# Optimization experiments

Hardware: AMD Instinct MI355X
Metric: run time of the kernel (lower is better)

Reference implementation:

```python
import jax, jax.numpy as jnp
import numpy as np

N = 8192
E = 131072
D_IN = 128
D_OUT = 128
EPS = 1e-5


def setup_inputs() -> dict:
    key = jax.random.key(0)
    k1, k2, k3, k4 = jax.random.split(key, 4)
    x = jax.random.normal(k1, (N, D_IN), dtype=jnp.float32)
    edge_index = jax.random.randint(k2, (2, E), 0, N, dtype=jnp.int64)
    weight = jax.random.normal(k3, (D_IN, D_OUT), dtype=jnp.float32)
    bias = jax.random.normal(k4, (D_OUT,), dtype=jnp.float32)
    return {"x": x, "edge_index": edge_index, "weight": weight, "bias": bias}


def reference(x, edge_index, weight, bias):
    n = x.shape[0]
    row, col = edge_index[0], edge_index[1]
    # dense adjacency build, exactly as the torch module does
    adj = jnp.zeros((n, n), dtype=x.dtype).at[row, col].set(1.0)
    adj = jnp.maximum(adj, adj.T)                      # symmetrize
    adj = adj + jnp.eye(n, dtype=x.dtype)              # self-loops (added, may yield 2 on diag)
    d_inv_sqrt = 1.0 / jnp.sqrt(adj.sum(axis=1) + EPS)  # [N]
    # D^{-1/2} A D^{-1/2} via broadcasting (same math as diag matmuls)
    norm_adj = d_inv_sqrt[:, None] * adj * d_inv_sqrt[None, :]
    out = norm_adj @ x            # [N, D_IN] aggregation
    out = out @ weight + bias     # [N, D_OUT]
    return out
```

## Files before the change

### kernel.cpp

```cpp
#include <hip/hip_runtime.h>
#include <stdint.h>

#define N_NODES 8192
#define NE      131072
#define DCH     128
#define WPR     256
#define MAXDEG  128
#define ZROW    8192
#define EPS     1e-5f

__global__ __launch_bounds__(256) void edge_kernel(const void* __restrict__ ei_raw,
                                                   uint32_t* __restrict__ bm) {
    int lane = threadIdx.x & 63;
    const long long* p64 = (const long long*)ei_raw;
    const int*       p32 = (const int*)ei_raw;
    bool is64 = __all((unsigned long long)p64[lane] < (unsigned long long)N_NODES);
    int e = blockIdx.x * 256 + threadIdx.x;
    int r, c;
    if (is64) { r = (int)p64[e]; c = (int)p64[NE + e]; }
    else      { r = p32[e];      c = p32[NE + e]; }
    atomicOr(&bm[r * WPR + (c >> 5)], 1u << (c & 31));
    atomicOr(&bm[c * WPR + (r >> 5)], 1u << (r & 31));
}

__global__ __launch_bounds__(256) void extract_kernel(const uint4* __restrict__ bm4,
                                                      float* __restrict__ dinv,
                                                      int* __restrict__ cnts,
                                                      uint16_t* __restrict__ nbr,
                                                      float* __restrict__ y) {
    if (blockIdx.x == 0 && threadIdx.x < DCH)
        y[(size_t)ZROW * DCH + threadIdx.x] = 0.0f;

    int lane = threadIdx.x & 63;
    int node = blockIdx.x * 4 + (threadIdx.x >> 6);
    uint4 w = bm4[(size_t)node * 64 + lane];
    int c = __popc(w.x) + __popc(w.y) + __popc(w.z) + __popc(w.w);
    int pre = c;
    #pragma unroll
    for (int d = 1; d < 64; d <<= 1) {
        int v = __shfl_up(pre, d);
        if (lane >= d) pre += v;
    }
    int tot  = __shfl(pre, 63);
    int excl = pre - c;
    int cnt  = tot > MAXDEG ? MAXDEG : tot;
    int kpad = (cnt + 7) & ~7;
    if (lane == 0) {
        dinv[node] = 1.0f / sqrtf((float)tot + 1.0f + EPS);
        cnts[node] = kpad;
    }
    uint32_t wd[4] = {w.x, w.y, w.z, w.w};
    int basebit = lane * 128;
    int o = excl;
    #pragma unroll
    for (int m = 0; m < 4; ++m) {
        uint32_t v = wd[m];
        while (v) {
            int b = __ffs(v) - 1; v &= v - 1;
            if (o < MAXDEG) nbr[(size_t)node * MAXDEG + o] = (uint16_t)(basebit + m * 32 + b);
            ++o;
        }
    }
    int p = cnt + lane;
    if (p < kpad) nbr[(size_t)node * MAXDEG + p] = (uint16_t)ZROW;
}

__global__ __launch_bounds__(256) void gemm_kernel(const float* __restrict__ X,
                                                   const float* __restrict__ W,
                                                   const float* __restrict__ dinv,
                                                   float* __restrict__ y) {
    __shared__ float sA[64][132];
    int t = threadIdx.x;
    int row0 = blockIdx.x * 64;
    int col0 = blockIdx.y * 64;
    {
        int k4 = t & 31;
        int r  = t >> 5;
        #pragma unroll
        for (int p = 0; p < 8; ++p) {
            float4 v = *(const float4*)&X[(size_t)(row0 + r + p * 8) * DCH + k4 * 4];
            *(float4*)&sA[r + p * 8][k4 * 4] = v;
        }
    }
    __syncthreads();

    int tx = t & 15, ty = t >> 4;
    int cg = col0 + tx * 4;
    int r0 = ty * 4;
    float acc[4][4] = {};
    #pragma unroll 4
    for (int k = 0; k < DCH; ++k) {
        float4 w = *(const float4*)&W[(size_t)k * DCH + cg];
        float a0 = sA[r0 + 0][k];
        float a1 = sA[r0 + 1][k];
        float a2 = sA[r0 + 2][k];
        float a3 = sA[r0 + 3][k];
        acc[0][0] += a0 * w.x; acc[0][1] += a0 * w.y; acc[0][2] += a0 * w.z; acc[0][3] += a0 * w.w;
        acc[1][0] += a1 * w.x; acc[1][1] += a1 * w.y; acc[1][2] += a1 * w.z; acc[1][3] += a1 * w.w;
        acc[2][0] += a2 * w.x; acc[2][1] += a2 * w.y; acc[2][2] += a2 * w.z; acc[2][3] += a2 * w.w;
        acc[3][0] += a3 * w.x; acc[3][1] += a3 * w.y; acc[3][2] += a3 * w.z; acc[3][3] += a3 * w.w;
    }
    #pragma unroll
    for (int i = 0; i < 4; ++i) {
        float d = dinv[row0 + r0 + i];
        float4 o;
        o.x = d * acc[i][0]; o.y = d * acc[i][1]; o.z = d * acc[i][2]; o.w = d * acc[i][3];
        *(float4*)&y[(size_t)(row0 + r0 + i) * DCH + cg] = o;
    }
}

__global__ __launch_bounds__(256) void aggregate_kernel(const uint16_t* __restrict__ nbr,
                                                        const float* __restrict__ dinv,
                                                        const int* __restrict__ cnts,
                                                        const float* __restrict__ y,
                                                        const float* __restrict__ bias,
                                                        float* __restrict__ out) {
    __shared__ uint32_t s_list[4][64];
    int w    = threadIdx.x >> 6;
    int lane = threadIdx.x & 63;
    int node = blockIdx.x * 4 + w;

    s_list[w][lane] = ((const uint32_t*)nbr)[(size_t)node * (MAXDEG / 2) + lane];
    const uint16_t* sl = (const uint16_t*)s_list[w];

    int   kpad = __builtin_amdgcn_readfirstlane(cnts[node]);
    float di   = dinv[node];
    const float2* y2 = (const float2*)y;

    float2 a0 = y2[(size_t)node * 64 + lane];
    float2 a1 = {0, 0}, a2 = {0, 0}, a3 = {0, 0};
    float2 a4 = {0, 0}, a5 = {0, 0}, a6 = {0, 0}, a7 = {0, 0};

    for (int k = 0; k < kpad; k += 8) {
        int j0 = __builtin_amdgcn_readfirstlane((int)sl[k + 0]);
        int j1 = __builtin_amdgcn_readfirstlane((int)sl[k + 1]);
        int j2 = __builtin_amdgcn_readfirstlane((int)sl[k + 2]);
        int j3 = __builtin_amdgcn_readfirstlane((int)sl[k + 3]);
        int j4 = __builtin_amdgcn_readfirstlane((int)sl[k + 4]);
        int j5 = __builtin_amdgcn_readfirstlane((int)sl[k + 5]);
        int j6 = __builtin_amdgcn_readfirstlane((int)sl[k + 6]);
        int j7 = __builtin_amdgcn_readfirstlane((int)sl[k + 7]);
        float2 q0 = y2[(size_t)j0 * 64 + lane];
        float2 q1 = y2[(size_t)j1 * 64 + lane];
        float2 q2 = y2[(size_t)j2 * 64 + lane];
        float2 q3 = y2[(size_t)j3 * 64 + lane];
        float2 q4 = y2[(size_t)j4 * 64 + lane];
        float2 q5 = y2[(size_t)j5 * 64 + lane];
        float2 q6 = y2[(size_t)j6 * 64 + lane];
        float2 q7 = y2[(size_t)j7 * 64 + lane];
        a0.x += q0.x; a0.y += q0.y;  a1.x += q1.x; a1.y += q1.y;
        a2.x += q2.x; a2.y += q2.y;  a3.x += q3.x; a3.y += q3.y;
        a4.x += q4.x; a4.y += q4.y;  a5.x += q5.x; a5.y += q5.y;
        a6.x += q6.x; a6.y += q6.y;  a7.x += q7.x; a7.y += q7.y;
    }

    float2 bb = ((const float2*)bias)[lane];
    float2 r;
    r.x = di * (((a0.x + a1.x) + (a2.x + a3.x)) + ((a4.x + a5.x) + (a6.x + a7.x))) + bb.x;
    r.y = di * (((a0.y + a1.y) + (a2.y + a3.y)) + ((a4.y + a5.y) + (a6.y + a7.y))) + bb.y;
    ((float2*)out)[(size_t)node * 64 + lane] = r;
}

extern "C" void kernel_launch(void* const* d_in, const int* in_sizes, int n_in,
                              void* d_out, int out_size, void* d_ws, size_t ws_size,
                              hipStream_t stream) {
    const float* xp  = (const float*)d_in[0];
    const void*  eip = d_in[1];
    const float* Wp  = (const float*)d_in[2];
    const float* bp  = (const float*)d_in[3];
    float*       op  = (float*)d_out;

    uint8_t* ws = (uint8_t*)d_ws;
    uint32_t* bmp   = (uint32_t*)ws;
    float*    dinvp = (float*)   (ws + (size_t)8 * 1024 * 1024);
    int*      cntp  = (int*)     (ws + (size_t)8 * 1024 * 1024 + 32 * 1024);
    uint16_t* nbrp  = (uint16_t*)(ws + (size_t)8 * 1024 * 1024 + 64 * 1024);
    float*    yp    = (float*)   (ws + (size_t)10 * 1024 * 1024 + 64 * 1024);

    hipMemsetAsync(bmp, 0, (size_t)N_NODES * WPR * sizeof(uint32_t), stream);
    edge_kernel<<<NE / 256, 256, 0, stream>>>(eip, bmp);
    extract_kernel<<<N_NODES / 4, 256, 0, stream>>>((const uint4*)bmp, dinvp, cntp, nbrp, yp);
    gemm_kernel<<<dim3(N_NODES / 64, 2), 256, 0, stream>>>(xp, Wp, dinvp, yp);
    aggregate_kernel<<<N_NODES / 4, 256, 0, stream>>>(nbrp, dinvp, cntp, yp, bp, op);
}
```

Before: 105.4 us.

## Fuse edge build with GEMM and fold neighbor extraction into aggregation

Edge scatter and the X@W GEMM now run in one launch, with disjoint block ranges, so they can overlap. Degrees are counted with atomics when a bit is newly set. The separate extract kernel is removed: aggregation reads the bitmap row, builds the neighbor list in shared memory and scales each neighbor by its own inverse sqrt degree. This cuts two launches and the nbr/dinv round trips, at the cost of extra degree atomics and per-neighbor degree loads and sqrt in the gather loop.

Result: slower. 118.4 us (+12.3%).

```diff
diff --git a/kernel.cpp b/kernel.cpp
--- a/kernel.cpp
+++ b/kernel.cpp
@@ -5,159 +5,137 @@
 #define NE      131072
 #define DCH     128
 #define WPR     256
-#define MAXDEG  128
-#define ZROW    8192
+#define MAXC    128
 #define EPS     1e-5f
 
-__global__ __launch_bounds__(256) void edge_kernel(const void* __restrict__ ei_raw,
-                                                   uint32_t* __restrict__ bm) {
-    int lane = threadIdx.x & 63;
-    const long long* p64 = (const long long*)ei_raw;
-    const int*       p32 = (const int*)ei_raw;
-    bool is64 = __all((unsigned long long)p64[lane] < (unsigned long long)N_NODES);
-    int e = blockIdx.x * 256 + threadIdx.x;
-    int r, c;
-    if (is64) { r = (int)p64[e]; c = (int)p64[NE + e]; }
-    else      { r = p32[e];      c = p32[NE + e]; }
-    atomicOr(&bm[r * WPR + (c >> 5)], 1u << (c & 31));
-    atomicOr(&bm[c * WPR + (r >> 5)], 1u << (r & 31));
+__global__ __launch_bounds__(256) void build_gemm_kernel(
+    const void*  __restrict__ ei_raw,
+    const float* __restrict__ X,
+    const float* __restrict__ W,
+    uint32_t* __restrict__ bm,
+    int*      __restrict__ deg,
+    float*    __restrict__ z)
+{
+    int t = threadIdx.x;
+    if (blockIdx.x < 512) {
+        int lane = t & 63;
+        const long long* p64 = (const long long*)ei_raw;
+        const int*       p32 = (const int*)ei_raw;
+        bool is64 = __all((unsigned long long)p64[lane] < (unsigned long long)N_NODES);
+        int e = blockIdx.x * 256 + t;
+        int r, c;
+        if (is64) { r = (int)p64[e]; c = (int)p64[NE + e]; }
+        else      { r = p32[e];      c = p32[NE + e]; }
+        uint32_t mc = 1u << (c & 31), mr = 1u << (r & 31);
+        uint32_t o1 = atomicOr(&bm[r * WPR + (c >> 5)], mc);
+        if (!(o1 & mc)) atomicAdd(&deg[r], 1);
+        uint32_t o2 = atomicOr(&bm[c * WPR + (r >> 5)], mr);
+        if (!(o2 & mr)) atomicAdd(&deg[c], 1);
+    } else {
+        __shared__ float sA[64][132];
+        int bx = blockIdx.x - 512;
+        int row0 = (bx >> 1) * 64;
+        int col0 = (bx & 1) * 64;
+        {
+            int k4 = t & 31;
+            int r  = t >> 5;
+            #pragma unroll
+            for (int p = 0; p < 8; ++p) {
+                float4 v = *(const float4*)&X[(size_t)(row0 + r + p * 8) * DCH + k4 * 4];
+                *(float4*)&sA[r + p * 8][k4 * 4] = v;
+            }
+        }
+        __syncthreads();
+        int tx = t & 15, ty = t >> 4;
+        int cg = col0 + tx * 4;
+        int r0 = ty * 4;
+        float acc[4][4] = {};
+        #pragma unroll 4
+        for (int k = 0; k < DCH; ++k) {
+            float4 w = *(const float4*)&W[(size_t)k * DCH + cg];
+            float a0 = sA[r0 + 0][k];
+            float a1 = sA[r0 + 1][k];
+            float a2 = sA[r0 + 2][k];
+            float a3 = sA[r0 + 3][k];
+            acc[0][0] += a0 * w.x; acc[0][1] += a0 * w.y; acc[0][2] += a0 * w.z; acc[0][3] += a0 * w.w;
+            acc[1][0] += a1 * w.x; acc[1][1] += a1 * w.y; acc[1][2] += a1 * w.z; acc[1][3] += a1 * w.w;
+            acc[2][0] += a2 * w.x; acc[2][1] += a2 * w.y; acc[2][2] += a2 * w.z; acc[2][3] += a2 * w.w;
+            acc[3][0] += a3 * w.x; acc[3][1] += a3 * w.y; acc[3][2] += a3 * w.z; acc[3][3] += a3 * w.w;
+        }
+        #pragma unroll
+        for (int i = 0; i < 4; ++i) {
+            float4 o;
+            o.x = acc[i][0]; o.y = acc[i][1]; o.z = acc[i][2]; o.w = acc[i][3];
+            *(float4*)&z[(size_t)(row0 + r0 + i) * DCH + cg] = o;
+        }
+    }
 }
 
-__global__ __launch_bounds__(256) void extract_kernel(const uint4* __restrict__ bm4,
-                                                      float* __restrict__ dinv,
-                                                      int* __restrict__ cnts,
-                                                      uint16_t* __restrict__ nbr,
-                                                      float* __restrict__ y) {
-    if (blockIdx.x == 0 && threadIdx.x < DCH)
-        y[(size_t)ZROW * DCH + threadIdx.x] = 0.0f;
+__global__ __launch_bounds__(256) void aggregate_kernel(
+    const uint4* __restrict__ bm4,
+    const int*   __restrict__ deg,
+    const float* __restrict__ z,
+    const float* __restrict__ bias,
+    float*       __restrict__ out)
+{
+    __shared__ uint16_t slist[4][MAXC];
+    int w    = threadIdx.x >> 6;
+    int lane = threadIdx.x & 63;
+    int node = blockIdx.x * 4 + w;
 
-    int lane = threadIdx.x & 63;
-    int node = blockIdx.x * 4 + (threadIdx.x >> 6);
-    uint4 w = bm4[(size_t)node * 64 + lane];
-    int c = __popc(w.x) + __popc(w.y) + __popc(w.z) + __popc(w.w);
+    uint4 b = bm4[(size_t)node * 64 + lane];
+    int c = __popc(b.x) + __popc(b.y) + __popc(b.z) + __popc(b.w);
     int pre = c;
     #pragma unroll
     for (int d = 1; d < 64; d <<= 1) {
         int v = __shfl_up(pre, d);
         if (lane >= d) pre += v;
     }
-    int tot  = __shfl(pre, 63);
-    int excl = pre - c;
-    int cnt  = tot > MAXDEG ? MAXDEG : tot;
-    int kpad = (cnt + 7) & ~7;
-    if (lane == 0) {
-        dinv[node] = 1.0f / sqrtf((float)tot + 1.0f + EPS);
-        cnts[node] = kpad;
-    }
-    uint32_t wd[4] = {w.x, w.y, w.z, w.w};
-    int basebit = lane * 128;
-    int o = excl;
-    #pragma unroll
-    for (int m = 0; m < 4; ++m) {
-        uint32_t v = wd[m];
-        while (v) {
-            int b = __ffs(v) - 1; v &= v - 1;
-            if (o < MAXDEG) nbr[(size_t)node * MAXDEG + o] = (uint16_t)(basebit + m * 32 + b);
-            ++o;
+    int total = __shfl(pre, 63);
+    int excl  = pre - c;
+
+    {
+        uint32_t wd[4] = {b.x, b.y, b.z, b.w};
+        int basebit = lane * 128;
+        int o = excl;
+        #pragma unroll
+        for (int m = 0; m < 4; ++m) {
+            uint32_t v = wd[m];
+            while (v) {
+                int bb = __ffs(v) - 1; v &= v - 1;
+                if (o < MAXC) slist[w][o] = (uint16_t)(basebit + m * 32 + bb);
+                ++o;
+            }
         }
     }
-    int p = cnt + lane;
-    if (p < kpad) nbr[(size_t)node * MAXDEG + p] = (uint16_t)ZROW;
-}
+    int cap  = total > MAXC ? MAXC : total;
+    int kpad = (cap + 7) & ~7;
+    int p = cap + lane;
+    if (p < kpad) slist[w][p] = (uint16_t)node;
 
-__global__ __launch_bounds__(256) void gemm_kernel(const float* __restrict__ X,
-                                                   const float* __restrict__ W,
-                                                   const float* __restrict__ dinv,
-                                                   float* __restrict__ y) {
-    __shared__ float sA[64][132];
-    int t = threadIdx.x;
-    int row0 = blockIdx.x * 64;
-    int col0 = blockIdx.y * 64;
-    {
-        int k4 = t & 31;
-        int r  = t >> 5;
-        #pragma unroll
-        for (int p = 0; p < 8; ++p) {
-            float4 v = *(const float4*)&X[(size_t)(row0 + r + p * 8) * DCH + k4 * 4];
-            *(float4*)&sA[r + p * 8][k4 * 4] = v;
-        }
-    }
-    __syncthreads();
+    const float2* z2 = (const float2*)z;
+    float dn = 1.0f / sqrtf((float)total + 1.0f + EPS);
 
-    int tx = t & 15, ty = t >> 4;
-    int cg = col0 + tx * 4;
-    int r0 = ty * 4;
-    float acc[4][4] = {};
-    #pragma unroll 4
-    for (int k = 0; k < DCH; ++k) {
-        float4 w = *(const float4*)&W[(size_t)k * DCH + cg];
-        float a0 = sA[r0 + 0][k];
-        float a1 = sA[r0 + 1][k];
-        float a2 = sA[r0 + 2][k];
-        float a3 = sA[r0 + 3][k];
-        acc[0][0] += a0 * w.x; acc[0][1] += a0 * w.y; acc[0][2] += a0 * w.z; acc[0][3] += a0 * w.w;
-        acc[1][0] += a1 * w.x; acc[1][1] += a1 * w.y; acc[1][2] += a1 * w.z; acc[1][3] += a1 * w.w;
-        acc[2][0] += a2 * w.x; acc[2][1] += a2 * w.y; acc[2][2] += a2 * w.z; acc[2][3] += a2 * w.w;
-        acc[3][0] += a3 * w.x; acc[3][1] += a3 * w.y; acc[3][2] += a3 * w.z; acc[3][3] += a3 * w.w;
-    }
-    #pragma unroll
-    for (int i = 0; i < 4; ++i) {
-        float d = dinv[row0 + r0 + i];
-        float4 o;
-        o.x = d * acc[i][0]; o.y = d * acc[i][1]; o.z = d * acc[i][2]; o.w = d * acc[i][3];
-        *(float4*)&y[(size_t)(row0 + r0 + i) * DCH + cg] = o;
-    }
-}
-
-__global__ __launch_bounds__(256) void aggregate_kernel(const uint16_t* __restrict__ nbr,
-                                                        const float* __restrict__ dinv,
-                                                        const int* __restrict__ cnts,
-                                                        const float* __restrict__ y,
-                                                        const float* __restrict__ bias,
-                                                        float* __restrict__ out) {
-    __shared__ uint32_t s_list[4][64];
-    int w    = threadIdx.x >> 6;
-    int lane = threadIdx.x & 63;
-    int node = blockIdx.x * 4 + w;
-
-    s_list[w][lane] = ((const uint32_t*)nbr)[(size_t)node * (MAXDEG / 2) + lane];
-    const uint16_t* sl = (const uint16_t*)s_list[w];
-
-    int   kpad = __builtin_amdgcn_readfirstlane(cnts[node]);
-    float di   = dinv[node];
-    const float2* y2 = (const float2*)y;
-
-    float2 a0 = y2[(size_t)node * 64 + lane];
-    float2 a1 = {0, 0}, a2 = {0, 0}, a3 = {0, 0};
-    float2 a4 = {0, 0}, a5 = {0, 0}, a6 = {0, 0}, a7 = {0, 0};
+    float2 self = z2[(size_t)node * 64 + lane];
+    float2 a0, a1 = {0,0}, a2 = {0,0}, a3 = {0,0}, a4 = {0,0}, a5 = {0,0}, a6 = {0,0}, a7 = {0,0};
+    a0.x = dn * self.x; a0.y = dn * self.y;
 
     for (int k = 0; k < kpad; k += 8) {
-        int j0 = __builtin_amdgcn_readfirstlane((int)sl[k + 0]);
-        int j1 = __builtin_amdgcn_readfirstlane((int)sl[k + 1]);
-        int j2 = __builtin_amdgcn_readfirstlane((int)sl[k + 2]);
-        int j3 = __builtin_amdgcn_readfirstlane((int)sl[k + 3]);
-        int j4 = __builtin_amdgcn_readfirstlane((int)sl[k + 4]);
-        int j5 = __builtin_amdgcn_readfirstlane((int)sl[k + 5]);
-        int j6 = __builtin_amdgcn_readfirstlane((int)sl[k + 6]);
-        int j7 = __builtin_amdgcn_readfirstlane((int)sl[k + 7]);
-        float2 q0 = y2[(size_t)j0 * 64 + lane];
-        float2 q1 = y2[(size_t)j1 * 64 + lane];
-        float2 q2 = y2[(size_t)j2 * 64 + lane];
-        float2 q3 = y2[(size_t)j3 * 64 + lane];
-        float2 q4 = y2[(size_t)j4 * 64 + lane];
-        float2 q5 = y2[(size_t)j5 * 64 + lane];
-        float2 q6 = y2[(size_t)j6 * 64 + lane];
-        float2 q7 = y2[(size_t)j7 * 64 + lane];
-        a0.x += q0.x; a0.y += q0.y;  a1.x += q1.x; a1.y += q1.y;
-        a2.x += q2.x; a2.y += q2.y;  a3.x += q3.x; a3.y += q3.y;
-        a4.x += q4.x; a4.y += q4.y;  a5.x += q5.x; a5.y += q5.y;
-        a6.x += q6.x; a6.y += q6.y;  a7.x += q7.x; a7.y += q7.y;
+        #define STEP(i, AX) {                                                        \
+            int idx = k + i;                                                         \
+            int j = __builtin_amdgcn_readfirstlane((int)slist[w][idx]);              \
+            float dj = (idx < cap) ? 1.0f / sqrtf((float)deg[j] + 1.0f + EPS) : 0.f; \
+            float2 q = z2[(size_t)j * 64 + lane];                                    \
+            AX.x += dj * q.x; AX.y += dj * q.y; }
+        STEP(0, a0) STEP(1, a1) STEP(2, a2) STEP(3, a3)
+        STEP(4, a4) STEP(5, a5) STEP(6, a6) STEP(7, a7)
+        #undef STEP
     }
 
     float2 bb = ((const float2*)bias)[lane];
     float2 r;
-    r.x = di * (((a0.x + a1.x) + (a2.x + a3.x)) + ((a4.x + a5.x) + (a6.x + a7.x))) + bb.x;
-    r.y = di * (((a0.y + a1.y) + (a2.y + a3.y)) + ((a4.y + a5.y) + (a6.y + a7.y))) + bb.y;
+    r.x = dn * (((a0.x + a1.x) + (a2.x + a3.x)) + ((a4.x + a5.x) + (a6.x + a7.x))) + bb.x;
+    r.y = dn * (((a0.y + a1.y) + (a2.y + a3.y)) + ((a4.y + a5.y) + (a6.y + a7.y))) + bb.y;
     ((float2*)out)[(size_t)node * 64 + lane] = r;
 }
 
@@ -171,15 +149,11 @@
     float*       op  = (float*)d_out;
 
     uint8_t* ws = (uint8_t*)d_ws;
-    uint32_t* bmp   = (uint32_t*)ws;
-    float*    dinvp = (float*)   (ws + (size_t)8 * 1024 * 1024);
-    int*      cntp  = (int*)     (ws + (size_t)8 * 1024 * 1024 + 32 * 1024);
-    uint16_t* nbrp  = (uint16_t*)(ws + (size_t)8 * 1024 * 1024 + 64 * 1024);
-    float*    yp    = (float*)   (ws + (size_t)10 * 1024 * 1024 + 64 * 1024);
+    uint32_t* bmp  = (uint32_t*)ws;
+    int*      degp = (int*)     (ws + (size_t)8 * 1024 * 1024);
+    float*    zp   = (float*)   (ws + (size_t)8 * 1024 * 1024 + 32 * 1024);
 
-    hipMemsetAsync(bmp, 0, (size_t)N_NODES * WPR * sizeof(uint32_t), stream);
-    edge_kernel<<<NE / 256, 256, 0, stream>>>(eip, bmp);
-    extract_kernel<<<N_NODES / 4, 256, 0, stream>>>((const uint4*)bmp, dinvp, cntp, nbrp, yp);
-    gemm_kernel<<<dim3(N_NODES / 64, 2), 256, 0, stream>>>(xp, Wp, dinvp, yp);
-    aggregate_kernel<<<N_NODES / 4, 256, 0, stream>>>(nbrp, dinvp, cntp, yp, bp, op);
+    hipMemsetAsync(bmp, 0, (size_t)8 * 1024 * 1024 + 32 * 1024, stream);
+    build_gemm_kernel<<<768, 256, 0, stream>>>(eip, xp, Wp, bmp, degp, zp);
+    aggregate_kernel<<<N_NODES / 4, 256, 0, stream>>>((const uint4*)bmp, degp, zp, bp, op);
 }
```
